# Kernel tuning notes

Measured on AMD Instinct MI355X. Metric: run time of the kernel, lower is better.

## Reference

```python
import jax, jax.numpy as jnp
import numpy as np

EMB = 1024
HEAD = 64  # emb_size // head_nb = 1024 // 16

def setup_inputs() -> dict:
    key = jax.random.key(0)
    kx, kq, kk, kv = jax.random.split(key, 4)
    x = jax.random.normal(kx, (8, 2048, EMB), dtype=jnp.float32)
    # torch nn.Linear(EMB, HEAD) weight has shape [HEAD, EMB]; y = x @ W.T
    s = 1.0 / np.sqrt(EMB)
    Wq = jax.random.uniform(kq, (HEAD, EMB), jnp.float32, -s, s)
    Wk = jax.random.uniform(kk, (HEAD, EMB), jnp.float32, -s, s)
    Wv = jax.random.uniform(kv, (HEAD, EMB), jnp.float32, -s, s)
    return {"x": x, "Wq": Wq, "Wk": Wk, "Wv": Wv}

def reference(x, Wq, Wk, Wv):
    B, T, C = x.shape
    q = jnp.einsum('btc,hc->bth', x, Wq)  # [B,T,H]
    k = jnp.einsum('btc,hc->bth', x, Wk)
    v = jnp.einsum('btc,hc->bth', x, Wv)
    scale = 1.0 / jnp.sqrt(jnp.float32(q.shape[-1]))
    wei = jnp.einsum('bth,bsh->bts', q, k) * scale  # [B,T,T]
    causal = jnp.tril(jnp.ones((T, T), dtype=bool))
    wei = jnp.where(causal, wei, -jnp.inf)
    wei = jax.nn.softmax(wei, axis=-1)
    # dropout is identity in eval mode
    out = jnp.einsum('bts,bsh->bth', wei, v)  # [B,T,H]
    return out
```

## Files before the change

### kernel.cpp

```cpp
#include <hip/hip_runtime.h>
#include <math.h>

#define SEQ  2048
#define NROW 16384
#define HEAD 64
#define EMB  1024

typedef __attribute__((ext_vector_type(8))) short short8;
typedef __attribute__((ext_vector_type(4))) float f32x4;

static __device__ __forceinline__ unsigned short f2bf(float f) {
    unsigned u = __builtin_bit_cast(unsigned, f);
    u += 0x7fffu + ((u >> 16) & 1u);
    return (unsigned short)(u >> 16);
}
static __device__ __forceinline__ float bf2f(unsigned short u) {
    unsigned v = (unsigned)u << 16;
    return __builtin_bit_cast(float, v);
}
static __device__ __forceinline__ ushort4 cvt4(float4 f) {
    ushort4 u;
    u.x = f2bf(f.x); u.y = f2bf(f.y); u.z = f2bf(f.z); u.w = f2bf(f.w);
    return u;
}

static __device__ __forceinline__ void gload_lds16(const void* g, void* l) {
    __builtin_amdgcn_global_load_lds(
        (const __attribute__((address_space(1))) unsigned int*)g,
        (__attribute__((address_space(3))) unsigned int*)l, 16, 0, 0);
}

__global__ __launch_bounds__(256) void wcvt_kernel(
    const float* __restrict__ Wq, const float* __restrict__ Wk,
    const float* __restrict__ Wv, unsigned short* __restrict__ Wb)
{
    const int idx = (blockIdx.x * 256 + threadIdx.x) * 4;
    const int h = idx >> 10;
    const float* src;
    if (h < 64)       src = Wq + idx;
    else if (h < 128) src = Wk + (idx - 65536);
    else              src = Wv + (idx - 131072);
    *(ushort4*)(Wb + idx) = cvt4(*(const float4*)src);
}

__global__ __launch_bounds__(256, 3) void qkv_mfma_kernel(
    const float* __restrict__ x, const unsigned short* __restrict__ Wb,
    unsigned short* __restrict__ qN, unsigned short* __restrict__ kN,
    unsigned short* __restrict__ vT)
{
    __shared__ unsigned short As[2][64][72];
    __shared__ unsigned short Bs[2][96 * 64];

    const int tid  = threadIdx.x;
    const int w    = tid >> 6;
    const int lane = tid & 63;
    const int col  = lane & 15;
    const int quad = lane >> 4;
    const int row0 = blockIdx.x * 64;
    const int ny   = blockIdx.y;
    const int arow = w * 16 + col;
    const int pq   = (quad ^ (col & 7)) * 8;

    const int ar_r = tid >> 4, ar_c = tid & 15;
    const float* xg = x + (size_t)(row0 + ar_r) * EMB + ar_c * 4;

    const int sr = lane >> 3, cc = (lane & 7) ^ sr;
    const unsigned short* bg = Wb + (size_t)(ny * 96) * EMB;

    {
        float4 fa[4];
#pragma unroll
        for (int j = 0; j < 4; ++j) fa[j] = *(const float4*)(xg + (size_t)(16 * j) * EMB);
#pragma unroll
        for (int j = 0; j < 4; ++j) *(ushort4*)&As[0][ar_r + 16 * j][ar_c * 4] = cvt4(fa[j]);
#pragma unroll
        for (int j = 0; j < 3; ++j) {
            const int r = (w * 3 + j) * 8 + sr;
            gload_lds16(bg + (size_t)r * EMB + cc * 8, &Bs[0][(w * 3 + j) * 8 * 64]);
        }
    }
    __syncthreads();

    f32x4 acc[6];
#pragma unroll
    for (int t = 0; t < 6; ++t) acc[t] = (f32x4){0.f, 0.f, 0.f, 0.f};

    float4 fa[4];
#pragma unroll 2
    for (int kt = 0; kt < 16; ++kt) {
        const int cur = kt & 1;
        if (kt + 1 < 16) {
            const int k0 = (kt + 1) * 64;
#pragma unroll
            for (int j = 0; j < 3; ++j) {
                const int r = (w * 3 + j) * 8 + sr;
                gload_lds16(bg + (size_t)r * EMB + k0 + cc * 8,
                            &Bs[cur ^ 1][(w * 3 + j) * 8 * 64]);
            }
#pragma unroll
            for (int j = 0; j < 4; ++j)
                fa[j] = *(const float4*)(xg + (size_t)(16 * j) * EMB + k0);
        }
#pragma unroll
        for (int ks = 0; ks < 2; ++ks) {
            short8 af = *(const short8*)&As[cur][arow][ks * 32 + quad * 8];
            const int po = pq ^ (ks * 32);
#pragma unroll
            for (int t = 0; t < 6; ++t) {
                short8 bf = *(const short8*)&Bs[cur][(t * 16 + col) * 64 + po];
                acc[t] = __builtin_amdgcn_mfma_f32_16x16x32_bf16(af, bf, acc[t], 0, 0, 0);
            }
        }
        if (kt + 1 < 16) {
#pragma unroll
            for (int j = 0; j < 4; ++j)
                *(ushort4*)&As[cur ^ 1][ar_r + 16 * j][ar_c * 4] = cvt4(fa[j]);
        }
        __syncthreads();
    }

    const int ro = row0 + w * 16 + quad * 4;
#pragma unroll
    for (int t = 0; t < 6; ++t) {
        const int hb = ny * 96 + 16 * t;
        const int h  = hb + col;
        if (hb < 64) {
#pragma unroll
            for (int r = 0; r < 4; ++r)
                qN[(size_t)(ro + r) * HEAD + h] = f2bf(acc[t][r] * 0.125f);
        } else if (hb < 128) {
#pragma unroll
            for (int r = 0; r < 4; ++r)
                kN[(size_t)(ro + r) * HEAD + (h - 64)] = f2bf(acc[t][r]);
        } else {
            ushort4 uv;
            uv.x = f2bf(acc[t][0]); uv.y = f2bf(acc[t][1]);
            uv.z = f2bf(acc[t][2]); uv.w = f2bf(acc[t][3]);
            *(ushort4*)(vT + (size_t)(h - 128) * NROW + ro) = uv;
        }
    }
}

__global__ __launch_bounds__(256, 3) void attn_kernel(
    const unsigned short* __restrict__ qN,
    const unsigned short* __restrict__ kN,
    const unsigned short* __restrict__ vT,
    unsigned short* __restrict__ op,
    float2* __restrict__ ml)
{
    __shared__ unsigned short Ks[2][64 * 64];
    __shared__ unsigned short Vs[2][64 * 64];
    __shared__ unsigned short Pl[4][32][72];

    const int qt   = 15 - (int)blockIdx.x;
    const int b    = blockIdx.y;
    const int p    = blockIdx.z;
    const int tid  = threadIdx.x;
    const int wv   = tid >> 6;
    const int lane = tid & 63;
    const int col  = lane & 15;
    const int quad = lane >> 4;

    const int q0   = qt * 128 + wv * 16;
    const int q0g  = b * SEQ + q0;
    const int Cb   = 2 * qt + 2;
    const int kt0  = (Cb * p) >> 2;
    const int kt1  = (Cb * (p + 1)) >> 2;
    const int ktp  = min(kt0, Cb - 1);

    const int sr = lane >> 3, cc = (lane & 7) ^ sr;
    const int pq = (quad ^ (col & 7)) * 8;
    const unsigned short* kgb = kN + (size_t)(b * SEQ) * HEAD;
    const int bcol = b * SEQ;

    const short8* qp0 = (const short8*)qN + (size_t)(q0g + col) * 8;
    const short8* qp1 = (const short8*)qN + (size_t)(q0g + 64 + col) * 8;
    short8 aq00 = qp0[quad], aq01 = qp0[quad + 4];
    short8 aq10 = qp1[quad], aq11 = qp1[quad + 4];

    f32x4 o[2][4];
    float l_i[2][4];
#pragma unroll
    for (int mi = 0; mi < 2; ++mi)
#pragma unroll
        for (int t = 0; t < 4; ++t) {
            o[mi][t] = (f32x4){0.f, 0.f, 0.f, 0.f};
            l_i[mi][t] = 0.f;
        }

#pragma unroll
    for (int j = 0; j < 2; ++j) {
        const int r = (wv * 2 + j) * 8 + sr;
        gload_lds16(kgb + (size_t)(ktp * 64 + r) * HEAD + cc * 8,
                    &Ks[0][(wv * 2 + j) * 8 * 64]);
        gload_lds16(vT + (size_t)r * NROW + bcol + ktp * 64 + cc * 8,
                    &Vs[0][(wv * 2 + j) * 8 * 64]);
    }
    __syncthreads();

    for (int kt = kt0; kt < kt1; ++kt) {
        const int cur = (kt - kt0) & 1;
        const int s0  = kt * 64;
        const bool dz = (kt >= Cb - 2);
        const bool m0 = (kt < Cb - 1);

        if (kt + 1 < kt1) {
#pragma unroll
            for (int j = 0; j < 2; ++j) {
                const int r = (wv * 2 + j) * 8 + sr;
                gload_lds16(kgb + (size_t)((kt + 1) * 64 + r) * HEAD + cc * 8,
                            &Ks[cur ^ 1][(wv * 2 + j) * 8 * 64]);
                gload_lds16(vT + (size_t)r * NROW + bcol + (kt + 1) * 64 + cc * 8,
                            &Vs[cur ^ 1][(wv * 2 + j) * 8 * 64]);
            }
        }

        f32x4 sv[2][4];
#pragma unroll
        for (int t = 0; t < 4; ++t) {
            sv[0][t] = (f32x4){0.f, 0.f, 0.f, 0.f};
            sv[1][t] = (f32x4){0.f, 0.f, 0.f, 0.f};
        }
#pragma unroll
        for (int t = 0; t < 4; ++t) {
            const int rb = (16 * t + col) * 64;
            short8 kf0 = *(const short8*)&Ks[cur][rb + pq];
            short8 kf1 = *(const short8*)&Ks[cur][rb + (pq ^ 32)];
            sv[1][t] = __builtin_amdgcn_mfma_f32_16x16x32_bf16(aq10, kf0, sv[1][t], 0, 0, 0);
            sv[1][t] = __builtin_amdgcn_mfma_f32_16x16x32_bf16(aq11, kf1, sv[1][t], 0, 0, 0);
            if (m0) {
                sv[0][t] = __builtin_amdgcn_mfma_f32_16x16x32_bf16(aq00, kf0, sv[0][t], 0, 0, 0);
                sv[0][t] = __builtin_amdgcn_mfma_f32_16x16x32_bf16(aq01, kf1, sv[0][t], 0, 0, 0);
            }
        }

#pragma unroll
        for (int mi = 0; mi < 2; ++mi) {
            if (mi == 0 && !m0) continue;
#pragma unroll
            for (int r = 0; r < 4; ++r) {
                const int grow = q0 + mi * 64 + quad * 4 + r;
                float ls = 0.f;
#pragma unroll
                for (int t = 0; t < 4; ++t) {
                    float e = __expf(sv[mi][t][r]);
                    if (dz && (s0 + 16 * t + col > grow)) e = 0.0f;
                    Pl[wv][mi * 16 + quad * 4 + r][16 * t + col] = f2bf(e);
                    ls += e;
                }
                l_i[mi][r] += ls;
            }
        }

        short8 pf00, pf01;
        if (m0) {
            pf00 = *(const short8*)&Pl[wv][col][quad * 8];
            pf01 = *(const short8*)&Pl[wv][col][quad * 8 + 32];
        }
        short8 pf10 = *(const short8*)&Pl[wv][16 + col][quad * 8];
        short8 pf11 = *(const short8*)&Pl[wv][16 + col][quad * 8 + 32];

#pragma unroll
        for (int tn = 0; tn < 4; ++tn) {
            const int rb = (16 * tn + col) * 64;
            short8 vf0 = *(const short8*)&Vs[cur][rb + pq];
            short8 vf1 = *(const short8*)&Vs[cur][rb + (pq ^ 32)];
            o[1][tn] = __builtin_amdgcn_mfma_f32_16x16x32_bf16(pf10, vf0, o[1][tn], 0, 0, 0);
            o[1][tn] = __builtin_amdgcn_mfma_f32_16x16x32_bf16(pf11, vf1, o[1][tn], 0, 0, 0);
            if (m0) {
                o[0][tn] = __builtin_amdgcn_mfma_f32_16x16x32_bf16(pf00, vf0, o[0][tn], 0, 0, 0);
                o[0][tn] = __builtin_amdgcn_mfma_f32_16x16x32_bf16(pf01, vf1, o[0][tn], 0, 0, 0);
            }
        }

        __syncthreads();
    }

#pragma unroll
    for (int mi = 0; mi < 2; ++mi) {
#pragma unroll
        for (int r = 0; r < 4; ++r) {
            float l = l_i[mi][r];
            l += __shfl_xor(l, 1, 16);
            l += __shfl_xor(l, 2, 16);
            l += __shfl_xor(l, 4, 16);
            l += __shfl_xor(l, 8, 16);
            l_i[mi][r] = l;
        }
        const int ro = q0g + mi * 64 + quad * 4;
#pragma unroll
        for (int tn = 0; tn < 4; ++tn)
#pragma unroll
            for (int r = 0; r < 4; ++r)
                op[((size_t)p * NROW + ro + r) * HEAD + 16 * tn + col] =
                    f2bf(o[mi][tn][r]);
        if (col == 0) {
#pragma unroll
            for (int r = 0; r < 4; ++r)
                ml[p * NROW + ro + r] = make_float2(0.0f, l_i[mi][r]);
        }
    }
}

__global__ __launch_bounds__(256) void merge_kernel(
    const unsigned short* __restrict__ op, const float2* __restrict__ ml,
    float* __restrict__ out)
{
    const int idx = blockIdx.x * 256 + threadIdx.x;
    const int row = idx >> 4;
    const int hc  = (idx & 15) * 4;

    float denom = 0.0f;
#pragma unroll
    for (int p = 0; p < 4; ++p) denom += ml[p * NROW + row].y;
    const float inv = 1.0f / denom;

    float4 r = make_float4(0.f, 0.f, 0.f, 0.f);
#pragma unroll
    for (int p = 0; p < 4; ++p) {
        ushort4 u = *(const ushort4*)(op + ((size_t)p * NROW + row) * HEAD + hc);
        r.x += bf2f(u.x);
        r.y += bf2f(u.y);
        r.z += bf2f(u.z);
        r.w += bf2f(u.w);
    }
    r.x *= inv; r.y *= inv; r.z *= inv; r.w *= inv;
    *(float4*)(out + (size_t)row * HEAD + hc) = r;
}

extern "C" void kernel_launch(void* const* d_in, const int* in_sizes, int n_in,
                              void* d_out, int out_size, void* d_ws, size_t ws_size,
                              hipStream_t stream)
{
    const float* x  = (const float*)d_in[0];
    const float* Wq = (const float*)d_in[1];
    const float* Wk = (const float*)d_in[2];
    const float* Wv = (const float*)d_in[3];

    char* w = (char*)d_ws;
    unsigned short* qN = (unsigned short*)w;
    unsigned short* kN = (unsigned short*)(w + (2u << 20));
    unsigned short* vT = (unsigned short*)(w + (4u << 20));
    unsigned short* Wb = (unsigned short*)(w + (6u << 20));
    unsigned short* op = (unsigned short*)(w + (6u << 20) + 393216);
    float2*         ml = (float2*)(w + (14u << 20) + 393216);
    float* out = (float*)d_out;

    wcvt_kernel<<<192, 256, 0, stream>>>(Wq, Wk, Wv, Wb);
    qkv_mfma_kernel<<<dim3(256, 2), 256, 0, stream>>>(x, Wb, qN, kN, vT);
    attn_kernel<<<dim3(16, 8, 4), 256, 0, stream>>>(qN, kN, vT, op, ml);
    merge_kernel<<<1024, 256, 0, stream>>>(op, ml, out);
}
```

Before: 138.2 us.

## Load x directly into MFMA fragments and triple-buffer weight tiles in QKV GEMM

The QKV projection kernel stops staging x through LDS. Each lane now loads its fp32 x fragment straight into registers, converts it to bf16 in-register and feeds it to the MFMA, with register double-buffering one k-step ahead. Weight tiles move to a three-deep LDS ring with prefetch two steps ahead, and explicit vmcnt waits plus raw s_barrier replace __syncthreads. Row tiles shrink to 32 (doubling the grid) with a 2x2 wave split and occupancy hint 4, trading less per-block reuse for more parallelism and relying on hand-counted vmcnt values being correct.

```diff
diff --git a/kernel.cpp b/kernel.cpp
--- a/kernel.cpp
+++ b/kernel.cpp
@@ -17,6 +17,12 @@
 static __device__ __forceinline__ float bf2f(unsigned short u) {
     unsigned v = (unsigned)u << 16;
     return __builtin_bit_cast(float, v);
+}
+static __device__ __forceinline__ short8 cvt8(float4 a, float4 b) {
+    short8 r;
+    r[0] = f2bf(a.x); r[1] = f2bf(a.y); r[2] = f2bf(a.z); r[3] = f2bf(a.w);
+    r[4] = f2bf(b.x); r[5] = f2bf(b.y); r[6] = f2bf(b.z); r[7] = f2bf(b.w);
+    return r;
 }
 static __device__ __forceinline__ ushort4 cvt4(float4 f) {
     ushort4 u;
@@ -43,86 +49,97 @@
     *(ushort4*)(Wb + idx) = cvt4(*(const float4*)src);
 }
 
-__global__ __launch_bounds__(256, 3) void qkv_mfma_kernel(
+__global__ __launch_bounds__(256, 4) void qkv_mfma_kernel(
     const float* __restrict__ x, const unsigned short* __restrict__ Wb,
     unsigned short* __restrict__ qN, unsigned short* __restrict__ kN,
     unsigned short* __restrict__ vT)
 {
-    __shared__ unsigned short As[2][64][72];
-    __shared__ unsigned short Bs[2][96 * 64];
+    __shared__ unsigned short Bs[3][96 * 64];
 
     const int tid  = threadIdx.x;
     const int w    = tid >> 6;
     const int lane = tid & 63;
     const int col  = lane & 15;
     const int quad = lane >> 4;
-    const int row0 = blockIdx.x * 64;
+    const int row0 = blockIdx.x * 32;
     const int ny   = blockIdx.y;
-    const int arow = w * 16 + col;
+    const int mi   = w >> 1;
+    const int ni   = w & 1;
     const int pq   = (quad ^ (col & 7)) * 8;
-
-    const int ar_r = tid >> 4, ar_c = tid & 15;
-    const float* xg = x + (size_t)(row0 + ar_r) * EMB + ar_c * 4;
 
     const int sr = lane >> 3, cc = (lane & 7) ^ sr;
     const unsigned short* bg = Wb + (size_t)(ny * 96) * EMB;
 
-    {
-        float4 fa[4];
-#pragma unroll
-        for (int j = 0; j < 4; ++j) fa[j] = *(const float4*)(xg + (size_t)(16 * j) * EMB);
-#pragma unroll
-        for (int j = 0; j < 4; ++j) *(ushort4*)&As[0][ar_r + 16 * j][ar_c * 4] = cvt4(fa[j]);
-#pragma unroll
-        for (int j = 0; j < 3; ++j) {
-            const int r = (w * 3 + j) * 8 + sr;
-            gload_lds16(bg + (size_t)r * EMB + cc * 8, &Bs[0][(w * 3 + j) * 8 * 64]);
-        }
-    }
-    __syncthreads();
-
-    f32x4 acc[6];
-#pragma unroll
-    for (int t = 0; t < 6; ++t) acc[t] = (f32x4){0.f, 0.f, 0.f, 0.f};
-
-    float4 fa[4];
-#pragma unroll 2
+    const float* xg = x + (size_t)(row0 + mi * 16 + col) * EMB + quad * 8;
+
+    float4 fa[2][2], fb[2][2];
+#pragma unroll
+    for (int ks = 0; ks < 2; ++ks) {
+        fa[ks][0] = *(const float4*)(xg + ks * 32);
+        fa[ks][1] = *(const float4*)(xg + ks * 32 + 4);
+    }
+    asm volatile("" ::: "memory");
+#pragma unroll
+    for (int j = 0; j < 3; ++j)
+        gload_lds16(bg + (size_t)((w * 3 + j) * 8 + sr) * EMB + cc * 8,
+                    &Bs[0][(w * 3 + j) * 8 * 64]);
+#pragma unroll
+    for (int j = 0; j < 3; ++j)
+        gload_lds16(bg + (size_t)((w * 3 + j) * 8 + sr) * EMB + 64 + cc * 8,
+                    &Bs[1][(w * 3 + j) * 8 * 64]);
+    asm volatile("s_waitcnt vmcnt(3)" ::: "memory");
+    __builtin_amdgcn_sched_barrier(0);
+    __builtin_amdgcn_s_barrier();
+
+    f32x4 acc[3];
+#pragma unroll
+    for (int t = 0; t < 3; ++t) acc[t] = (f32x4){0.f, 0.f, 0.f, 0.f};
+
+#pragma unroll
     for (int kt = 0; kt < 16; ++kt) {
-        const int cur = kt & 1;
+        const int cur = kt % 3;
         if (kt + 1 < 16) {
-            const int k0 = (kt + 1) * 64;
-#pragma unroll
-            for (int j = 0; j < 3; ++j) {
-                const int r = (w * 3 + j) * 8 + sr;
-                gload_lds16(bg + (size_t)r * EMB + k0 + cc * 8,
-                            &Bs[cur ^ 1][(w * 3 + j) * 8 * 64]);
-            }
-#pragma unroll
-            for (int j = 0; j < 4; ++j)
-                fa[j] = *(const float4*)(xg + (size_t)(16 * j) * EMB + k0);
+#pragma unroll
+            for (int ks = 0; ks < 2; ++ks) {
+                fb[ks][0] = *(const float4*)(xg + (kt + 1) * 64 + ks * 32);
+                fb[ks][1] = *(const float4*)(xg + (kt + 1) * 64 + ks * 32 + 4);
+            }
+        }
+        if (kt + 2 < 16) {
+            const int nb = (kt + 2) % 3;
+#pragma unroll
+            for (int j = 0; j < 3; ++j)
+                gload_lds16(bg + (size_t)((w * 3 + j) * 8 + sr) * EMB
+                                + (kt + 2) * 64 + cc * 8,
+                            &Bs[nb][(w * 3 + j) * 8 * 64]);
         }
 #pragma unroll
         for (int ks = 0; ks < 2; ++ks) {
-            short8 af = *(const short8*)&As[cur][arow][ks * 32 + quad * 8];
+            short8 af = cvt8(fa[ks][0], fa[ks][1]);
             const int po = pq ^ (ks * 32);
 #pragma unroll
-            for (int t = 0; t < 6; ++t) {
-                short8 bf = *(const short8*)&Bs[cur][(t * 16 + col) * 64 + po];
+            for (int t = 0; t < 3; ++t) {
+                short8 bf = *(const short8*)
+                    &Bs[cur][(ni * 48 + t * 16 + col) * 64 + po];
                 acc[t] = __builtin_amdgcn_mfma_f32_16x16x32_bf16(af, bf, acc[t], 0, 0, 0);
             }
         }
+#pragma unroll
+        for (int ks = 0; ks < 2; ++ks) {
+            fa[ks][0] = fb[ks][0]; fa[ks][1] = fb[ks][1];
+        }
         if (kt + 1 < 16) {
-#pragma unroll
-            for (int j = 0; j < 4; ++j)
-                *(ushort4*)&As[cur ^ 1][ar_r + 16 * j][ar_c * 4] = cvt4(fa[j]);
-        }
-        __syncthreads();
-    }
-
-    const int ro = row0 + w * 16 + quad * 4;
-#pragma unroll
-    for (int t = 0; t < 6; ++t) {
-        const int hb = ny * 96 + 16 * t;
+            if (kt + 2 < 16) asm volatile("s_waitcnt vmcnt(7)" ::: "memory");
+            else             asm volatile("s_waitcnt vmcnt(4)" ::: "memory");
+            __builtin_amdgcn_sched_barrier(0);
+            __builtin_amdgcn_s_barrier();
+        }
+    }
+
+    const int ro = row0 + mi * 16 + quad * 4;
+#pragma unroll
+    for (int t = 0; t < 3; ++t) {
+        const int hb = ny * 96 + ni * 48 + 16 * t;
         const int h  = hb + col;
         if (hb < 64) {
 #pragma unroll
@@ -347,7 +364,7 @@
     float* out = (float*)d_out;
 
     wcvt_kernel<<<192, 256, 0, stream>>>(Wq, Wk, Wv, Wb);
-    qkv_mfma_kernel<<<dim3(256, 2), 256, 0, stream>>>(x, Wb, qN, kN, vT);
+    qkv_mfma_kernel<<<dim3(512, 2), 256, 0, stream>>>(x, Wb, qN, kN, vT);
     attn_kernel<<<dim3(16, 8, 4), 256, 0, stream>>>(qN, kN, vT, op, ml);
     merge_kernel<<<1024, 256, 0, stream>>>(op, ml, out);
 }
```

Result: slower. 157.0 us (+13.7%).

## Compute all 192 QKV columns per block to read x once

Applied to the files above, without the earlier changes.

The QKV projection grid changes from 256x2 blocks of 256 threads, each computing 96 output columns, to 256 blocks of 512 threads that each compute all 192 columns. Eight waves are arranged 2x4 over a 64x192 tile. Each x row tile is now loaded and converted to bf16 once instead of twice, which halves the fp32 x reads from global memory. The cost is a larger LDS footprint for the weight buffer, fewer blocks in the grid, and lower occupancy bounds.

```diff
diff --git a/kernel.cpp b/kernel.cpp
--- a/kernel.cpp
+++ b/kernel.cpp
@@ -43,13 +43,13 @@
     *(ushort4*)(Wb + idx) = cvt4(*(const float4*)src);
 }
 
-__global__ __launch_bounds__(256, 3) void qkv_mfma_kernel(
+__global__ __launch_bounds__(512, 2) void qkv_mfma_kernel(
     const float* __restrict__ x, const unsigned short* __restrict__ Wb,
     unsigned short* __restrict__ qN, unsigned short* __restrict__ kN,
     unsigned short* __restrict__ vT)
 {
     __shared__ unsigned short As[2][64][72];
-    __shared__ unsigned short Bs[2][96 * 64];
+    __shared__ unsigned short Bs[2][192 * 64];
 
     const int tid  = threadIdx.x;
     const int w    = tid >> 6;
@@ -57,35 +57,38 @@
     const int col  = lane & 15;
     const int quad = lane >> 4;
     const int row0 = blockIdx.x * 64;
-    const int ny   = blockIdx.y;
-    const int arow = w * 16 + col;
+    const int wm   = w >> 2;
+    const int wn   = w & 3;
     const int pq   = (quad ^ (col & 7)) * 8;
 
     const int ar_r = tid >> 4, ar_c = tid & 15;
     const float* xg = x + (size_t)(row0 + ar_r) * EMB + ar_c * 4;
 
     const int sr = lane >> 3, cc = (lane & 7) ^ sr;
-    const unsigned short* bg = Wb + (size_t)(ny * 96) * EMB;
+    const unsigned short* bg = Wb;
 
     {
-        float4 fa[4];
-#pragma unroll
-        for (int j = 0; j < 4; ++j) fa[j] = *(const float4*)(xg + (size_t)(16 * j) * EMB);
-#pragma unroll
-        for (int j = 0; j < 4; ++j) *(ushort4*)&As[0][ar_r + 16 * j][ar_c * 4] = cvt4(fa[j]);
+        float4 fa[2];
+#pragma unroll
+        for (int j = 0; j < 2; ++j) fa[j] = *(const float4*)(xg + (size_t)(32 * j) * EMB);
+#pragma unroll
+        for (int j = 0; j < 2; ++j) *(ushort4*)&As[0][ar_r + 32 * j][ar_c * 4] = cvt4(fa[j]);
 #pragma unroll
         for (int j = 0; j < 3; ++j) {
-            const int r = (w * 3 + j) * 8 + sr;
-            gload_lds16(bg + (size_t)r * EMB + cc * 8, &Bs[0][(w * 3 + j) * 8 * 64]);
+            const int c = w * 3 + j;
+            gload_lds16(bg + (size_t)(c * 8 + sr) * EMB + cc * 8,
+                        &Bs[0][c * 8 * 64]);
         }
     }
     __syncthreads();
 
-    f32x4 acc[6];
-#pragma unroll
-    for (int t = 0; t < 6; ++t) acc[t] = (f32x4){0.f, 0.f, 0.f, 0.f};
-
-    float4 fa[4];
+    f32x4 acc[2][3];
+#pragma unroll
+    for (int mf = 0; mf < 2; ++mf)
+#pragma unroll
+        for (int t = 0; t < 3; ++t) acc[mf][t] = (f32x4){0.f, 0.f, 0.f, 0.f};
+
+    float4 fa[2];
 #pragma unroll 2
     for (int kt = 0; kt < 16; ++kt) {
         const int cur = kt & 1;
@@ -93,50 +96,56 @@
             const int k0 = (kt + 1) * 64;
 #pragma unroll
             for (int j = 0; j < 3; ++j) {
-                const int r = (w * 3 + j) * 8 + sr;
-                gload_lds16(bg + (size_t)r * EMB + k0 + cc * 8,
-                            &Bs[cur ^ 1][(w * 3 + j) * 8 * 64]);
-            }
-#pragma unroll
-            for (int j = 0; j < 4; ++j)
-                fa[j] = *(const float4*)(xg + (size_t)(16 * j) * EMB + k0);
+                const int c = w * 3 + j;
+                gload_lds16(bg + (size_t)(c * 8 + sr) * EMB + k0 + cc * 8,
+                            &Bs[cur ^ 1][c * 8 * 64]);
+            }
+#pragma unroll
+            for (int j = 0; j < 2; ++j)
+                fa[j] = *(const float4*)(xg + (size_t)(32 * j) * EMB + k0);
         }
 #pragma unroll
         for (int ks = 0; ks < 2; ++ks) {
-            short8 af = *(const short8*)&As[cur][arow][ks * 32 + quad * 8];
+            short8 af0 = *(const short8*)&As[cur][wm * 32 + col][ks * 32 + quad * 8];
+            short8 af1 = *(const short8*)&As[cur][wm * 32 + 16 + col][ks * 32 + quad * 8];
             const int po = pq ^ (ks * 32);
 #pragma unroll
-            for (int t = 0; t < 6; ++t) {
-                short8 bf = *(const short8*)&Bs[cur][(t * 16 + col) * 64 + po];
-                acc[t] = __builtin_amdgcn_mfma_f32_16x16x32_bf16(af, bf, acc[t], 0, 0, 0);
+            for (int t = 0; t < 3; ++t) {
+                short8 bf = *(const short8*)
+                    &Bs[cur][(wn * 48 + t * 16 + col) * 64 + po];
+                acc[0][t] = __builtin_amdgcn_mfma_f32_16x16x32_bf16(af0, bf, acc[0][t], 0, 0, 0);
+                acc[1][t] = __builtin_amdgcn_mfma_f32_16x16x32_bf16(af1, bf, acc[1][t], 0, 0, 0);
             }
         }
         if (kt + 1 < 16) {
 #pragma unroll
-            for (int j = 0; j < 4; ++j)
-                *(ushort4*)&As[cur ^ 1][ar_r + 16 * j][ar_c * 4] = cvt4(fa[j]);
+            for (int j = 0; j < 2; ++j)
+                *(ushort4*)&As[cur ^ 1][ar_r + 32 * j][ar_c * 4] = cvt4(fa[j]);
         }
         __syncthreads();
     }
 
-    const int ro = row0 + w * 16 + quad * 4;
-#pragma unroll
-    for (int t = 0; t < 6; ++t) {
-        const int hb = ny * 96 + 16 * t;
-        const int h  = hb + col;
-        if (hb < 64) {
-#pragma unroll
-            for (int r = 0; r < 4; ++r)
-                qN[(size_t)(ro + r) * HEAD + h] = f2bf(acc[t][r] * 0.125f);
-        } else if (hb < 128) {
-#pragma unroll
-            for (int r = 0; r < 4; ++r)
-                kN[(size_t)(ro + r) * HEAD + (h - 64)] = f2bf(acc[t][r]);
-        } else {
-            ushort4 uv;
-            uv.x = f2bf(acc[t][0]); uv.y = f2bf(acc[t][1]);
-            uv.z = f2bf(acc[t][2]); uv.w = f2bf(acc[t][3]);
-            *(ushort4*)(vT + (size_t)(h - 128) * NROW + ro) = uv;
+#pragma unroll
+    for (int mf = 0; mf < 2; ++mf) {
+        const int ro = row0 + wm * 32 + mf * 16 + quad * 4;
+#pragma unroll
+        for (int t = 0; t < 3; ++t) {
+            const int hb = wn * 48 + 16 * t;
+            const int h  = hb + col;
+            if (hb < 64) {
+#pragma unroll
+                for (int r = 0; r < 4; ++r)
+                    qN[(size_t)(ro + r) * HEAD + h] = f2bf(acc[mf][t][r] * 0.125f);
+            } else if (hb < 128) {
+#pragma unroll
+                for (int r = 0; r < 4; ++r)
+                    kN[(size_t)(ro + r) * HEAD + (h - 64)] = f2bf(acc[mf][t][r]);
+            } else {
+                ushort4 uv;
+                uv.x = f2bf(acc[mf][t][0]); uv.y = f2bf(acc[mf][t][1]);
+                uv.z = f2bf(acc[mf][t][2]); uv.w = f2bf(acc[mf][t][3]);
+                *(ushort4*)(vT + (size_t)(h - 128) * NROW + ro) = uv;
+            }
         }
     }
 }
@@ -347,7 +356,7 @@
     float* out = (float*)d_out;
 
     wcvt_kernel<<<192, 256, 0, stream>>>(Wq, Wk, Wv, Wb);
-    qkv_mfma_kernel<<<dim3(256, 2), 256, 0, stream>>>(x, Wb, qN, kN, vT);
+    qkv_mfma_kernel<<<256, 512, 0, stream>>>(x, Wb, qN, kN, vT);
     attn_kernel<<<dim3(16, 8, 4), 256, 0, stream>>>(qN, kN, vT, op, ml);
     merge_kernel<<<1024, 256, 0, stream>>>(op, ml, out);
 }
```

Result: no change. 137.4 us (median of 2 runs) (-0.5%).

## Drop LDS staging in QKV projection; pre-pack weights into MFMA fragment layout

Applied to the files above, without the earlier changes.

The weight-conversion kernel now writes the bf16 weights in a k8-major layout that matches MFMA B-operand fragments. The QKV projection then loads x and the weights directly from global memory into registers, with no LDS double buffering and no barriers. Each wave now computes all 192 output heads for 16 rows, so x is read once instead of twice across the two y-blocks. The cost is that weight fragments are re-read from global or L2 by every wave, accumulator register pressure grows to 12 tiles, and the loop loses its explicit prefetch pipelining.

```diff
diff --git a/kernel.cpp b/kernel.cpp
--- a/kernel.cpp
+++ b/kernel.cpp
@@ -18,6 +18,12 @@
     unsigned v = (unsigned)u << 16;
     return __builtin_bit_cast(float, v);
 }
+static __device__ __forceinline__ short8 cvt8(float4 a, float4 b) {
+    short8 r;
+    r[0] = f2bf(a.x); r[1] = f2bf(a.y); r[2] = f2bf(a.z); r[3] = f2bf(a.w);
+    r[4] = f2bf(b.x); r[5] = f2bf(b.y); r[6] = f2bf(b.z); r[7] = f2bf(b.w);
+    return r;
+}
 static __device__ __forceinline__ ushort4 cvt4(float4 f) {
     ushort4 u;
     u.x = f2bf(f.x); u.y = f2bf(f.y); u.z = f2bf(f.z); u.w = f2bf(f.w);
@@ -32,97 +38,55 @@
 
 __global__ __launch_bounds__(256) void wcvt_kernel(
     const float* __restrict__ Wq, const float* __restrict__ Wk,
-    const float* __restrict__ Wv, unsigned short* __restrict__ Wb)
-{
-    const int idx = (blockIdx.x * 256 + threadIdx.x) * 4;
-    const int h = idx >> 10;
+    const float* __restrict__ Wv, unsigned short* __restrict__ Wp)
+{
+    const int u = blockIdx.x * 256 + threadIdx.x;
+    const int k8 = u / 192;
+    const int h  = u - k8 * 192;
     const float* src;
-    if (h < 64)       src = Wq + idx;
-    else if (h < 128) src = Wk + (idx - 65536);
-    else              src = Wv + (idx - 131072);
-    *(ushort4*)(Wb + idx) = cvt4(*(const float4*)src);
-}
-
-__global__ __launch_bounds__(256, 3) void qkv_mfma_kernel(
-    const float* __restrict__ x, const unsigned short* __restrict__ Wb,
+    if (h < 64)       src = Wq + (size_t)h * EMB;
+    else if (h < 128) src = Wk + (size_t)(h - 64) * EMB;
+    else              src = Wv + (size_t)(h - 128) * EMB;
+    float4 a = *(const float4*)(src + k8 * 8);
+    float4 b = *(const float4*)(src + k8 * 8 + 4);
+    *(short8*)(Wp + (size_t)u * 8) = cvt8(a, b);
+}
+
+__global__ __launch_bounds__(256) void qkv_mfma_kernel(
+    const float* __restrict__ x, const unsigned short* __restrict__ Wp,
     unsigned short* __restrict__ qN, unsigned short* __restrict__ kN,
     unsigned short* __restrict__ vT)
 {
-    __shared__ unsigned short As[2][64][72];
-    __shared__ unsigned short Bs[2][96 * 64];
-
     const int tid  = threadIdx.x;
-    const int w    = tid >> 6;
     const int lane = tid & 63;
     const int col  = lane & 15;
     const int quad = lane >> 4;
-    const int row0 = blockIdx.x * 64;
-    const int ny   = blockIdx.y;
-    const int arow = w * 16 + col;
-    const int pq   = (quad ^ (col & 7)) * 8;
-
-    const int ar_r = tid >> 4, ar_c = tid & 15;
-    const float* xg = x + (size_t)(row0 + ar_r) * EMB + ar_c * 4;
-
-    const int sr = lane >> 3, cc = (lane & 7) ^ sr;
-    const unsigned short* bg = Wb + (size_t)(ny * 96) * EMB;
-
-    {
-        float4 fa[4];
-#pragma unroll
-        for (int j = 0; j < 4; ++j) fa[j] = *(const float4*)(xg + (size_t)(16 * j) * EMB);
-#pragma unroll
-        for (int j = 0; j < 4; ++j) *(ushort4*)&As[0][ar_r + 16 * j][ar_c * 4] = cvt4(fa[j]);
-#pragma unroll
-        for (int j = 0; j < 3; ++j) {
-            const int r = (w * 3 + j) * 8 + sr;
-            gload_lds16(bg + (size_t)r * EMB + cc * 8, &Bs[0][(w * 3 + j) * 8 * 64]);
-        }
-    }
-    __syncthreads();
-
-    f32x4 acc[6];
-#pragma unroll
-    for (int t = 0; t < 6; ++t) acc[t] = (f32x4){0.f, 0.f, 0.f, 0.f};
-
-    float4 fa[4];
+    const int wid  = blockIdx.x * 4 + (tid >> 6);
+
+    const float* xg  = x + (size_t)(wid * 16 + col) * EMB + quad * 8;
+    const short8* wp = (const short8*)Wp;
+
+    f32x4 acc[12];
+#pragma unroll
+    for (int t = 0; t < 12; ++t) acc[t] = (f32x4){0.f, 0.f, 0.f, 0.f};
+
 #pragma unroll 2
-    for (int kt = 0; kt < 16; ++kt) {
-        const int cur = kt & 1;
-        if (kt + 1 < 16) {
-            const int k0 = (kt + 1) * 64;
-#pragma unroll
-            for (int j = 0; j < 3; ++j) {
-                const int r = (w * 3 + j) * 8 + sr;
-                gload_lds16(bg + (size_t)r * EMB + k0 + cc * 8,
-                            &Bs[cur ^ 1][(w * 3 + j) * 8 * 64]);
-            }
-#pragma unroll
-            for (int j = 0; j < 4; ++j)
-                fa[j] = *(const float4*)(xg + (size_t)(16 * j) * EMB + k0);
-        }
-#pragma unroll
-        for (int ks = 0; ks < 2; ++ks) {
-            short8 af = *(const short8*)&As[cur][arow][ks * 32 + quad * 8];
-            const int po = pq ^ (ks * 32);
-#pragma unroll
-            for (int t = 0; t < 6; ++t) {
-                short8 bf = *(const short8*)&Bs[cur][(t * 16 + col) * 64 + po];
-                acc[t] = __builtin_amdgcn_mfma_f32_16x16x32_bf16(af, bf, acc[t], 0, 0, 0);
-            }
-        }
-        if (kt + 1 < 16) {
-#pragma unroll
-            for (int j = 0; j < 4; ++j)
-                *(ushort4*)&As[cur ^ 1][ar_r + 16 * j][ar_c * 4] = cvt4(fa[j]);
-        }
-        __syncthreads();
-    }
-
-    const int ro = row0 + w * 16 + quad * 4;
-#pragma unroll
-    for (int t = 0; t < 6; ++t) {
-        const int hb = ny * 96 + 16 * t;
+    for (int k8 = 0; k8 < 128; k8 += 4) {
+        float4 a0 = *(const float4*)(xg + k8 * 8);
+        float4 a1 = *(const float4*)(xg + k8 * 8 + 4);
+        short8 af = cvt8(a0, a1);
+        const int ub = (k8 + quad) * 192 + col;
+#pragma unroll
+        for (int t = 0; t < 12; ++t) {
+            short8 bf = wp[ub + t * 16];
+            acc[t] = __builtin_amdgcn_mfma_f32_16x16x32_bf16(af, bf, acc[t], 0, 0, 0);
+        }
+    }
+
+    const int ro = wid * 16 + quad * 4;
+#pragma unroll
+    for (int t = 0; t < 12; ++t) {
+        const int hb = t * 16;
         const int h  = hb + col;
         if (hb < 64) {
 #pragma unroll
@@ -341,13 +305,13 @@
     unsigned short* qN = (unsigned short*)w;
     unsigned short* kN = (unsigned short*)(w + (2u << 20));
     unsigned short* vT = (unsigned short*)(w + (4u << 20));
-    unsigned short* Wb = (unsigned short*)(w + (6u << 20));
+    unsigned short* Wp = (unsigned short*)(w + (6u << 20));
     unsigned short* op = (unsigned short*)(w + (6u << 20) + 393216);
     float2*         ml = (float2*)(w + (14u << 20) + 393216);
     float* out = (float*)d_out;
 
-    wcvt_kernel<<<192, 256, 0, stream>>>(Wq, Wk, Wv, Wb);
-    qkv_mfma_kernel<<<dim3(256, 2), 256, 0, stream>>>(x, Wb, qN, kN, vT);
+    wcvt_kernel<<<96, 256, 0, stream>>>(Wq, Wk, Wv, Wp);
+    qkv_mfma_kernel<<<256, 256, 0, stream>>>(x, Wp, qN, kN, vT);
     attn_kernel<<<dim3(16, 8, 4), 256, 0, stream>>>(qN, kN, vT, op, ml);
     merge_kernel<<<1024, 256, 0, stream>>>(op, ml, out);
 }
```

Measured after the change: 235.4 us. 1.7x slower.
